# Kernel optimization log

Hardware: AMD Instinct MI355X
Metric: run time of the kernel (lower is better)

Reference implementation:

```python
import jax, jax.numpy as jnp
import numpy as np

B, S, D, H = 8, 1024, 512, 12
HS = D // H  # 42 (head_size; 12*42 = 504 concat width, as in the original)


def setup_inputs() -> dict:
    key = jax.random.key(0)
    ks = jax.random.split(key, 12)
    sd = 0.02
    return {
        "embedded_patches": jax.random.normal(ks[0], (B, S, D), dtype=jnp.float32),
        # stacked per-head projections (12 independent Linear(D, HS, bias=False))
        "wk": jax.random.normal(ks[1], (H, D, HS), dtype=jnp.float32) * sd,
        "wq": jax.random.normal(ks[2], (H, D, HS), dtype=jnp.float32) * sd,
        "wv": jax.random.normal(ks[3], (H, D, HS), dtype=jnp.float32) * sd,
        "w_proj": jax.random.normal(ks[4], (H * HS, D), dtype=jnp.float32) * sd,  # [504, 512]
        "b_proj": jnp.zeros((D,), dtype=jnp.float32),
        # shared LayerNorm (same params used for both norms, as in the original)
        "gamma": jnp.ones((D,), dtype=jnp.float32),
        "beta": jnp.zeros((D,), dtype=jnp.float32),
        "w1": jax.random.normal(ks[5], (D, 4 * D), dtype=jnp.float32) * sd,
        "b1": jnp.zeros((4 * D,), dtype=jnp.float32),
        "w2": jax.random.normal(ks[6], (4 * D, D), dtype=jnp.float32) * sd,
        "b2": jnp.zeros((D,), dtype=jnp.float32),
    }


def _layernorm(x, gamma, beta, eps=1e-5):
    mu = jnp.mean(x, axis=-1, keepdims=True)
    var = jnp.var(x, axis=-1, keepdims=True)
    return (x - mu) * jax.lax.rsqrt(var + eps) * gamma + beta


def reference(embedded_patches, wk, wq, wv, w_proj, b_proj, gamma, beta, w1, b1, w2, b2):
    x = embedded_patches
    n1 = _layernorm(x, gamma, beta)
    # per-head projections, vectorized over heads: [B,S,D] x [H,D,E] -> [B,H,S,E]
    q = jnp.einsum('bsd,hde->bhse', n1, wq)
    k = jnp.einsum('bsd,hde->bhse', n1, wk)
    v = jnp.einsum('bsd,hde->bhse', n1, wv)
    scale = HS ** -0.5
    wei = jax.nn.softmax(jnp.einsum('bhse,bhte->bhst', q, k) * scale, axis=-1)
    out = jnp.einsum('bhst,bhte->bhse', wei, v)        # [B,H,S,E]
    out = out.transpose(0, 2, 1, 3).reshape(B, S, H * HS)  # concat heads -> [B,S,504]
    attn = out @ w_proj + b_proj                       # [B,S,D]
    # original quirk: takes batch element 0 and broadcasts against residual
    first_added = attn[0] + x                          # [S,D] + [B,S,D] -> [B,S,D]
    n2 = _layernorm(first_added, gamma, beta)
    h = jax.nn.gelu(n2 @ w1 + b1, approximate=False)   # torch nn.GELU default = exact erf
    ff = h @ w2 + b2
    return ff + first_added
```

## Files before the change

kernel.cpp:

```cpp
#include <hip/hip_runtime.h>
#include <hip/hip_bf16.h>
#include <stdint.h>


typedef unsigned short u16;
typedef __attribute__((ext_vector_type(8))) short short8;
typedef __attribute__((ext_vector_type(4))) float f32x4;

__device__ __forceinline__ u16 f2bf(float f) {
  union { float f; unsigned u; } x; x.f = f;
  return (u16)((x.u + 0x7FFFu + ((x.u >> 16) & 1u)) >> 16);
}
__device__ __forceinline__ float bf2f(u16 u) {
  union { unsigned u; float f; } x; x.u = ((unsigned)u) << 16;
  return x.f;
}

__device__ __forceinline__ void gload_lds16(const u16* g, u16* l) {
  __builtin_amdgcn_global_load_lds(
      (__attribute__((address_space(1))) void*)g,
      (__attribute__((address_space(3))) void*)l, 16, 0, 0);
}

__device__ __forceinline__ float wred_sum(float v) {
#pragma unroll
  for (int off = 32; off > 0; off >>= 1) v += __shfl_xor(v, off, 64);
  return v;
}
__device__ __forceinline__ float wred_max(float v) {
#pragma unroll
  for (int off = 32; off > 0; off >>= 1) v = fmaxf(v, __shfl_xor(v, off, 64));
  return v;
}

#define MFMA16x16(a, b, c) __builtin_amdgcn_mfma_f32_16x16x32_bf16(a, b, c, 0, 0, 0)

enum { EP_BF16 = 0, EP_PV = 1, EP_F32B = 2, EP_GELU = 3, EP_OUT = 4 };

template <int EP>
__launch_bounds__(256, 4)
__global__ void gemm2(const u16* __restrict__ A, int lda, long sAz,
                      const u16* __restrict__ Bt, int ldb, long sBz,
                      void* __restrict__ Cv, int ldc, long sCz,
                      int K, const float* __restrict__ bias,
                      const float* __restrict__ aux) {
  __shared__ u16 lA[2][128 * 32];
  __shared__ u16 lB[2][128 * 32];
  const int z = blockIdx.z;
  const u16* Ab = A + (long)z * sAz;
  const u16* Bb = Bt + (long)z * sBz;
  const int m0 = blockIdx.x * 128;
  const int n0 = blockIdx.y * 128;
  const int tid = threadIdx.x;
  const int w = tid >> 6;
  const int l = tid & 63;
  const int wr = w >> 1;
  const int wc = w & 1;
  const int NT = K >> 5;

  f32x4 acc[4][4];
#pragma unroll
  for (int i = 0; i < 4; ++i)
#pragma unroll
    for (int j = 0; j < 4; ++j) acc[i][j] = (f32x4){0.f, 0.f, 0.f, 0.f};

  const int srow = w * 32 + (l >> 2);
  const int sk = (l & 3) * 8;
  const u16* ga0 = Ab + (long)(m0 + srow) * lda + sk;
  const u16* ga1 = Ab + (long)(m0 + srow + 16) * lda + sk;
  const u16* gb0 = Bb + (long)(n0 + srow) * ldb + sk;
  const u16* gb1 = Bb + (long)(n0 + srow + 16) * ldb + sk;
  const int dOff = w * 1024;

  const int aoff = (wr * 64 + (l & 15)) * 32 + (l >> 4) * 8;
  const int boff = (wc * 64 + (l & 15)) * 32 + (l >> 4) * 8;

  gload_lds16(ga0, &lA[0][dOff]);
  gload_lds16(ga1, &lA[0][dOff + 512]);
  gload_lds16(gb0, &lB[0][dOff]);
  gload_lds16(gb1, &lB[0][dOff + 512]);
  __syncthreads();

  int buf = 0;
  for (int t = 0; t < NT; ++t) {
    short8 af[4], bfv[4];
#pragma unroll
    for (int mi = 0; mi < 4; ++mi)
      af[mi] = *(const short8*)&lA[buf][aoff + mi * 16 * 32];
#pragma unroll
    for (int ni = 0; ni < 4; ++ni)
      bfv[ni] = *(const short8*)&lB[buf][boff + ni * 16 * 32];
    if (t + 1 < NT) {
      const int k0 = (t + 1) * 32;
      const int nb = buf ^ 1;
      gload_lds16(ga0 + k0, &lA[nb][dOff]);
      gload_lds16(ga1 + k0, &lA[nb][dOff + 512]);
      gload_lds16(gb0 + k0, &lB[nb][dOff]);
      gload_lds16(gb1 + k0, &lB[nb][dOff + 512]);
    }
#pragma unroll
    for (int mi = 0; mi < 4; ++mi)
#pragma unroll
      for (int ni = 0; ni < 4; ++ni)
        acc[mi][ni] = MFMA16x16(af[mi], bfv[ni], acc[mi][ni]);
    __syncthreads();
    buf ^= 1;
  }

  const int rbase = m0 + wr * 64 + (l >> 4) * 4;
  const int cbase = n0 + wc * 64 + (l & 15);
#pragma unroll
  for (int mi = 0; mi < 4; ++mi) {
#pragma unroll
    for (int ni = 0; ni < 4; ++ni) {
#pragma unroll
      for (int j = 0; j < 4; ++j) {
        const int row = rbase + mi * 16 + j;
        const int col = cbase + ni * 16;
        const float v = acc[mi][ni][j];
        if (EP == EP_BF16) {
          ((u16*)Cv)[(long)z * sCz + (long)row * ldc + col] = f2bf(v);
        } else if (EP == EP_PV) {
          if (col < 42) {
            const float iv = aux[z * 1024 + row];
            ((u16*)Cv)[(long)row * ldc + z * 42 + col] = f2bf(v * iv);
          }
        } else if (EP == EP_F32B) {
          ((float*)Cv)[(long)row * ldc + col] = v + bias[col];
        } else if (EP == EP_GELU) {
          const float tt = v + bias[col];
          const float g = 0.5f * tt * (1.0f + erff(tt * 0.70710678118654752f));
          ((u16*)Cv)[(long)row * ldc + col] = f2bf(g);
        } else {
          ((float*)Cv)[(long)row * ldc + col] =
              v + bias[col] + aux[(long)row * ldc + col];
        }
      }
    }
  }
}

__global__ void ln1_kernel(const float* __restrict__ x,
                           const float* __restrict__ gamma,
                           const float* __restrict__ beta,
                           u16* __restrict__ n1) {
  __shared__ float red[16];
  const int s = blockIdx.x;
  const int t = threadIdx.x;
  const float* row = x + (long)s * 512;
  const float v0 = row[t];
  const float v1 = row[t + 256];
  float sum = wred_sum(v0 + v1);
  float sq = wred_sum(v0 * v0 + v1 * v1);
  if ((t & 63) == 0) { red[t >> 6] = sum; red[8 + (t >> 6)] = sq; }
  __syncthreads();
  sum = red[0] + red[1] + red[2] + red[3];
  sq = red[8] + red[9] + red[10] + red[11];
  const float mu = sum * (1.0f / 512.0f);
  const float rstd = rsqrtf(sq * (1.0f / 512.0f) - mu * mu + 1e-5f);
  n1[(long)s * 512 + t] = f2bf((v0 - mu) * rstd * gamma[t] + beta[t]);
  n1[(long)s * 512 + t + 256] =
      f2bf((v1 - mu) * rstd * gamma[t + 256] + beta[t + 256]);
}

__global__ void ln2_kernel(const float* __restrict__ x,
                           const float* __restrict__ aproj,
                           const float* __restrict__ gamma,
                           const float* __restrict__ beta,
                           float* __restrict__ fa, u16* __restrict__ n2) {
  __shared__ float red[16];
  const int r = blockIdx.x;
  const int t = threadIdx.x;
  const int s = r & 1023;
  const float* xr = x + (long)r * 512;
  const float* ar = aproj + (long)s * 512;
  const float v0 = xr[t] + ar[t];
  const float v1 = xr[t + 256] + ar[t + 256];
  fa[(long)r * 512 + t] = v0;
  fa[(long)r * 512 + t + 256] = v1;
  float sum = wred_sum(v0 + v1);
  float sq = wred_sum(v0 * v0 + v1 * v1);
  if ((t & 63) == 0) { red[t >> 6] = sum; red[8 + (t >> 6)] = sq; }
  __syncthreads();
  sum = red[0] + red[1] + red[2] + red[3];
  sq = red[8] + red[9] + red[10] + red[11];
  const float mu = sum * (1.0f / 512.0f);
  const float rstd = rsqrtf(sq * (1.0f / 512.0f) - mu * mu + 1e-5f);
  n2[(long)r * 512 + t] = f2bf((v0 - mu) * rstd * gamma[t] + beta[t]);
  n2[(long)r * 512 + t + 256] =
      f2bf((v1 - mu) * rstd * gamma[t + 256] + beta[t + 256]);
}

__global__ void softmax_kernel(u16* __restrict__ SP, float* __restrict__ invl) {
  __shared__ float red[16];
  const long row = blockIdx.x;
  u16* p = SP + row * 1024;
  const int t = threadIdx.x;
  uint2 u = ((const uint2*)p)[t];
  const float s0 = bf2f((u16)(u.x & 0xffff));
  const float s1 = bf2f((u16)(u.x >> 16));
  const float s2 = bf2f((u16)(u.y & 0xffff));
  const float s3 = bf2f((u16)(u.y >> 16));
  float m = wred_max(fmaxf(fmaxf(s0, s1), fmaxf(s2, s3)));
  if ((t & 63) == 0) red[t >> 6] = m;
  __syncthreads();
  m = fmaxf(fmaxf(red[0], red[1]), fmaxf(red[2], red[3]));
  const float e0 = __expf(s0 - m), e1 = __expf(s1 - m);
  const float e2 = __expf(s2 - m), e3 = __expf(s3 - m);
  float sum = wred_sum(e0 + e1 + e2 + e3);
  if ((t & 63) == 0) red[8 + (t >> 6)] = sum;
  __syncthreads();
  sum = red[8] + red[9] + red[10] + red[11];
  if (t == 0) invl[row] = 1.0f / sum;
  uint2 o;
  o.x = (unsigned)f2bf(e0) | ((unsigned)f2bf(e1) << 16);
  o.y = (unsigned)f2bf(e2) | ((unsigned)f2bf(e3) << 16);
  ((uint2*)p)[t] = o;
}

__global__ void prep_qkv_kernel(const float* __restrict__ wq,
                                const float* __restrict__ wk,
                                u16* __restrict__ BtQKV, float scale) {
  const int i = blockIdx.x * 256 + threadIdx.x;
  const int n = i >> 9, d = i & 511;
  const int pq = n / 768;
  const int h = (n % 768) >> 6;
  const int e = n & 63;
  float v = 0.f;
  if (e < 42) {
    v = (pq ? wk : wq)[((long)h * 512 + d) * 42 + e];
    if (!pq) v *= scale;
  }
  BtQKV[i] = f2bf(v);
}
__global__ void prep_wvT_kernel(const float* __restrict__ wv,
                                u16* __restrict__ wvT) {
  const int i = blockIdx.x * 256 + threadIdx.x;
  const int r = i >> 9, d = i & 511;
  const int h = r >> 7, e = r & 127;
  wvT[i] = f2bf(e < 42 ? wv[((long)h * 512 + d) * 42 + e] : 0.f);
}
__global__ void prep_proj_kernel(const float* __restrict__ wp,
                                 u16* __restrict__ BtP) {
  const int i = blockIdx.x * 256 + threadIdx.x;
  const int n = i >> 9, k = i & 511;
  BtP[i] = f2bf(k < 504 ? wp[(long)k * 512 + n] : 0.f);
}
__global__ void prep_w1_kernel(const float* __restrict__ w1,
                               u16* __restrict__ Bt1) {
  const int i = blockIdx.x * 256 + threadIdx.x;
  const int n = i >> 9, k = i & 511;
  Bt1[i] = f2bf(w1[(long)k * 2048 + n]);
}
__global__ void prep_w2_kernel(const float* __restrict__ w2,
                               u16* __restrict__ Bt2) {
  const int i = blockIdx.x * 256 + threadIdx.x;
  const int n = i >> 11, k = i & 2047;
  Bt2[i] = f2bf(w2[(long)k * 512 + n]);
}
__global__ void zero_u16_kernel(u16* __restrict__ p) {
  p[blockIdx.x * 256 + threadIdx.x] = 0;
}

extern "C" void kernel_launch(void* const* d_in, const int* in_sizes, int n_in,
                              void* d_out, int out_size, void* d_ws,
                              size_t ws_size, hipStream_t stream) {
  const float* x = (const float*)d_in[0];
  const float* wk = (const float*)d_in[1];
  const float* wq = (const float*)d_in[2];
  const float* wv = (const float*)d_in[3];
  const float* w_proj = (const float*)d_in[4];
  const float* b_proj = (const float*)d_in[5];
  const float* gamma = (const float*)d_in[6];
  const float* beta = (const float*)d_in[7];
  const float* w1 = (const float*)d_in[8];
  const float* b1 = (const float*)d_in[9];
  const float* w2 = (const float*)d_in[10];
  const float* b2 = (const float*)d_in[11];

  char* base = (char*)d_ws;
  size_t off = 0;
  auto alloc = [&](size_t bytes) -> void* {
    void* p = base + off;
    off += (bytes + 255) & ~(size_t)255;
    return p;
  };
  u16* n1 = (u16*)alloc(1024L * 512 * 2);
  u16* qkvc = (u16*)alloc(1024L * 1536 * 2);
  u16* SP = (u16*)alloc(12L * 1024 * 1024 * 2);
  u16* wvT = (u16*)alloc(1536L * 512 * 2);
  u16* vt = (u16*)alloc(1536L * 1024 * 2);
  u16* cat = (u16*)alloc(1024L * 512 * 2);
  float* aproj = (float*)alloc(1024L * 512 * 4);
  float* fa = (float*)alloc(8192L * 512 * 4);
  u16* n2 = (u16*)alloc(8192L * 512 * 2);
  u16* hbuf = (u16*)alloc(8192L * 2048 * 2);
  u16* BtQKV = (u16*)alloc(1536L * 512 * 2);
  u16* BtP = (u16*)alloc(512L * 512 * 2);
  u16* Bt1 = (u16*)alloc(2048L * 512 * 2);
  u16* Bt2 = (u16*)alloc(512L * 2048 * 2);
  float* invl = (float*)alloc(12L * 1024 * 4);
  (void)ws_size; (void)in_sizes; (void)n_in; (void)out_size;

  const float scale = 0.15430334996209191f;

  prep_qkv_kernel<<<3072, 256, 0, stream>>>(wq, wk, BtQKV, scale);
  prep_wvT_kernel<<<3072, 256, 0, stream>>>(wv, wvT);
  prep_proj_kernel<<<1024, 256, 0, stream>>>(w_proj, BtP);
  prep_w1_kernel<<<4096, 256, 0, stream>>>(w1, Bt1);
  prep_w2_kernel<<<4096, 256, 0, stream>>>(w2, Bt2);
  zero_u16_kernel<<<2048, 256, 0, stream>>>(cat);
  ln1_kernel<<<1024, 256, 0, stream>>>(x, gamma, beta, n1);

  gemm2<EP_BF16><<<dim3(8, 12, 1), 256, 0, stream>>>(
      n1, 512, 0, BtQKV, 512, 0, qkvc, 1536, 0, 512, nullptr, nullptr);
  gemm2<EP_BF16><<<dim3(12, 8, 1), 256, 0, stream>>>(
      wvT, 512, 0, n1, 512, 0, vt, 1024, 0, 512, nullptr, nullptr);
  gemm2<EP_BF16><<<dim3(8, 8, 12), 256, 0, stream>>>(
      qkvc, 1536, 64, qkvc + 768, 1536, 64, SP, 1024, 1024L * 1024, 64,
      nullptr, nullptr);
  softmax_kernel<<<12288, 256, 0, stream>>>(SP, invl);
  gemm2<EP_PV><<<dim3(8, 1, 12), 256, 0, stream>>>(
      SP, 1024, 1024L * 1024, vt, 1024, 128L * 1024, cat, 512, 0, 1024,
      nullptr, invl);
  gemm2<EP_F32B><<<dim3(8, 4, 1), 256, 0, stream>>>(
      cat, 512, 0, BtP, 512, 0, aproj, 512, 0, 512, b_proj, nullptr);
  ln2_kernel<<<8192, 256, 0, stream>>>(x, aproj, gamma, beta, fa, n2);
  gemm2<EP_GELU><<<dim3(64, 16, 1), 256, 0, stream>>>(
      n2, 512, 0, Bt1, 512, 0, hbuf, 2048, 0, 512, b1, nullptr);
  gemm2<EP_OUT><<<dim3(64, 4, 1), 256, 0, stream>>>(
      hbuf, 2048, 0, Bt2, 2048, 0, d_out, 512, 0, 2048, b2, fa);
}
```

Baseline: 188.3 us.

## Split-K for PV and MLP2 GEMMs, swizzle LDS, tiled weight transposes

Applies an XOR swizzle to the LDS layout in the shared GEMM to reduce bank conflicts. Splits the PV GEMM four ways along K and the final MLP GEMM two ways along K to raise the block count on undersized grids, with new combine kernels that sum the partials and apply the epilogue (invl scaling, bias, residual). Replaces the strided weight-prep kernels with an LDS-tiled transpose for coalesced access. The cost is extra fp32 partial traffic and more kernel launches; the MLP2 partials are written at the start of d_ws and could alias the other allocations.

Result: no change. 185.1 us (-1.7%).

```diff
diff --git a/kernel.cpp b/kernel.cpp
--- a/kernel.cpp
+++ b/kernel.cpp
@@ -35,7 +35,8 @@
 
 #define MFMA16x16(a, b, c) __builtin_amdgcn_mfma_f32_16x16x32_bf16(a, b, c, 0, 0, 0)
 
-enum { EP_BF16 = 0, EP_PV = 1, EP_F32B = 2, EP_GELU = 3, EP_OUT = 4 };
+enum { EP_BF16 = 0, EP_PV = 1, EP_F32B = 2, EP_GELU = 3, EP_OUT = 4,
+       EP_PART = 5, EP_PVPART = 6 };
 
 template <int EP>
 __launch_bounds__(256, 4)
@@ -47,8 +48,15 @@
   __shared__ u16 lA[2][128 * 32];
   __shared__ u16 lB[2][128 * 32];
   const int z = blockIdx.z;
-  const u16* Ab = A + (long)z * sAz;
-  const u16* Bb = Bt + (long)z * sBz;
+  const u16* Ab;
+  const u16* Bb;
+  if (EP == EP_PVPART) {
+    Ab = A + (long)(z >> 2) * sAz + (z & 3) * 256;
+    Bb = Bt + (long)(z >> 2) * sBz + (z & 3) * 256;
+  } else {
+    Ab = A + (long)z * sAz;
+    Bb = Bt + (long)z * sBz;
+  }
   const int m0 = blockIdx.x * 128;
   const int n0 = blockIdx.y * 128;
   const int tid = threadIdx.x;
@@ -65,15 +73,16 @@
     for (int j = 0; j < 4; ++j) acc[i][j] = (f32x4){0.f, 0.f, 0.f, 0.f};
 
   const int srow = w * 32 + (l >> 2);
-  const int sk = (l & 3) * 8;
+  const int sk = ((l & 3) ^ ((l >> 3) & 3)) * 8;
   const u16* ga0 = Ab + (long)(m0 + srow) * lda + sk;
   const u16* ga1 = Ab + (long)(m0 + srow + 16) * lda + sk;
   const u16* gb0 = Bb + (long)(n0 + srow) * ldb + sk;
   const u16* gb1 = Bb + (long)(n0 + srow + 16) * ldb + sk;
   const int dOff = w * 1024;
 
-  const int aoff = (wr * 64 + (l & 15)) * 32 + (l >> 4) * 8;
-  const int boff = (wc * 64 + (l & 15)) * 32 + (l >> 4) * 8;
+  const int gphys = ((l >> 4) ^ ((l >> 1) & 3)) * 8;
+  const int aoff = (wr * 64 + (l & 15)) * 32 + gphys;
+  const int boff = (wc * 64 + (l & 15)) * 32 + gphys;
 
   gload_lds16(ga0, &lA[0][dOff]);
   gload_lds16(ga1, &lA[0][dOff + 512]);
@@ -131,13 +140,41 @@
           const float tt = v + bias[col];
           const float g = 0.5f * tt * (1.0f + erff(tt * 0.70710678118654752f));
           ((u16*)Cv)[(long)row * ldc + col] = f2bf(g);
-        } else {
+        } else if (EP == EP_OUT) {
           ((float*)Cv)[(long)row * ldc + col] =
               v + bias[col] + aux[(long)row * ldc + col];
+        } else {
+          ((float*)Cv)[(long)z * sCz + (long)row * ldc + col] = v;
         }
       }
     }
   }
+}
+
+__global__ void combine_mlp2_kernel(const float* __restrict__ p,
+                                    const float* __restrict__ fa,
+                                    const float* __restrict__ b2,
+                                    float* __restrict__ out) {
+  const long i = (long)blockIdx.x * 256 + threadIdx.x;
+  const f32x4 a = ((const f32x4*)p)[i];
+  const f32x4 b = ((const f32x4*)(p + 8192L * 512))[i];
+  const f32x4 f = ((const f32x4*)fa)[i];
+  const f32x4 bb = ((const f32x4*)b2)[i & 127];
+  ((f32x4*)out)[i] = a + b + f + bb;
+}
+
+__global__ void combine_pv_kernel(const float* __restrict__ part,
+                                  const float* __restrict__ invl,
+                                  u16* __restrict__ cat) {
+  const int blk = blockIdx.x;
+  const int h = blk >> 10;
+  const int row = blk & 1023;
+  const int e = threadIdx.x;
+  if (e >= 42) return;
+  const long base = (long)(h * 4) * 131072 + row * 128 + e;
+  float v = part[base] + part[base + 131072] + part[base + 2 * 131072] +
+            part[base + 3 * 131072];
+  cat[(long)row * 512 + h * 42 + e] = f2bf(v * invl[h * 1024 + row]);
 }
 
 __global__ void ln1_kernel(const float* __restrict__ x,
@@ -240,24 +277,37 @@
   const int h = r >> 7, e = r & 127;
   wvT[i] = f2bf(e < 42 ? wv[((long)h * 512 + d) * 42 + e] : 0.f);
 }
-__global__ void prep_proj_kernel(const float* __restrict__ wp,
-                                 u16* __restrict__ BtP) {
-  const int i = blockIdx.x * 256 + threadIdx.x;
-  const int n = i >> 9, k = i & 511;
-  BtP[i] = f2bf(k < 504 ? wp[(long)k * 512 + n] : 0.f);
-}
-__global__ void prep_w1_kernel(const float* __restrict__ w1,
-                               u16* __restrict__ Bt1) {
-  const int i = blockIdx.x * 256 + threadIdx.x;
-  const int n = i >> 9, k = i & 511;
-  Bt1[i] = f2bf(w1[(long)k * 2048 + n]);
-}
-__global__ void prep_w2_kernel(const float* __restrict__ w2,
-                               u16* __restrict__ Bt2) {
-  const int i = blockIdx.x * 256 + threadIdx.x;
-  const int n = i >> 11, k = i & 2047;
-  Bt2[i] = f2bf(w2[(long)k * 512 + n]);
-}
+
+__global__ void transpose_bf16_kernel(const float* __restrict__ in,
+                                      u16* __restrict__ out, int N, int Kin,
+                                      int Kpad) {
+  __shared__ float tile[64][65];
+  const int n0 = blockIdx.x * 64;
+  const int k0 = blockIdx.y * 64;
+  const int t = threadIdx.x;
+  const int tc = t & 63;
+  const int tr = t >> 6;
+#pragma unroll
+  for (int r = 0; r < 16; ++r) {
+    const int kr = tr * 16 + r;
+    const int kg = k0 + kr;
+    tile[kr][tc] = (kg < Kin) ? in[(long)kg * N + n0 + tc] : 0.f;
+  }
+  __syncthreads();
+  const int nr0 = t >> 4;
+  const int kc = (t & 15) * 4;
+#pragma unroll
+  for (int p = 0; p < 4; ++p) {
+    const int nr = nr0 + p * 16;
+    ushort4 v;
+    v.x = f2bf(tile[kc + 0][nr]);
+    v.y = f2bf(tile[kc + 1][nr]);
+    v.z = f2bf(tile[kc + 2][nr]);
+    v.w = f2bf(tile[kc + 3][nr]);
+    *(ushort4*)&out[(long)(n0 + nr) * Kpad + k0 + kc] = v;
+  }
+}
+
 __global__ void zero_u16_kernel(u16* __restrict__ p) {
   p[blockIdx.x * 256 + threadIdx.x] = 0;
 }
@@ -300,15 +350,17 @@
   u16* Bt1 = (u16*)alloc(2048L * 512 * 2);
   u16* Bt2 = (u16*)alloc(512L * 2048 * 2);
   float* invl = (float*)alloc(12L * 1024 * 4);
+  float* pvpart = (float*)alloc(48L * 1024 * 128 * 4);
+  float* part = (float*)d_ws;
   (void)ws_size; (void)in_sizes; (void)n_in; (void)out_size;
 
   const float scale = 0.15430334996209191f;
 
   prep_qkv_kernel<<<3072, 256, 0, stream>>>(wq, wk, BtQKV, scale);
   prep_wvT_kernel<<<3072, 256, 0, stream>>>(wv, wvT);
-  prep_proj_kernel<<<1024, 256, 0, stream>>>(w_proj, BtP);
-  prep_w1_kernel<<<4096, 256, 0, stream>>>(w1, Bt1);
-  prep_w2_kernel<<<4096, 256, 0, stream>>>(w2, Bt2);
+  transpose_bf16_kernel<<<dim3(8, 8), 256, 0, stream>>>(w_proj, BtP, 512, 504, 512);
+  transpose_bf16_kernel<<<dim3(32, 8), 256, 0, stream>>>(w1, Bt1, 2048, 512, 512);
+  transpose_bf16_kernel<<<dim3(8, 32), 256, 0, stream>>>(w2, Bt2, 512, 2048, 2048);
   zero_u16_kernel<<<2048, 256, 0, stream>>>(cat);
   ln1_kernel<<<1024, 256, 0, stream>>>(x, gamma, beta, n1);
 
@@ -320,14 +372,17 @@
       qkvc, 1536, 64, qkvc + 768, 1536, 64, SP, 1024, 1024L * 1024, 64,
       nullptr, nullptr);
   softmax_kernel<<<12288, 256, 0, stream>>>(SP, invl);
-  gemm2<EP_PV><<<dim3(8, 1, 12), 256, 0, stream>>>(
-      SP, 1024, 1024L * 1024, vt, 1024, 128L * 1024, cat, 512, 0, 1024,
-      nullptr, invl);
+  gemm2<EP_PVPART><<<dim3(8, 1, 48), 256, 0, stream>>>(
+      SP, 1024, 1024L * 1024, vt, 1024, 128L * 1024, pvpart, 128,
+      1024L * 128, 256, nullptr, nullptr);
+  combine_pv_kernel<<<12288, 64, 0, stream>>>(pvpart, invl, cat);
   gemm2<EP_F32B><<<dim3(8, 4, 1), 256, 0, stream>>>(
       cat, 512, 0, BtP, 512, 0, aproj, 512, 0, 512, b_proj, nullptr);
   ln2_kernel<<<8192, 256, 0, stream>>>(x, aproj, gamma, beta, fa, n2);
   gemm2<EP_GELU><<<dim3(64, 16, 1), 256, 0, stream>>>(
       n2, 512, 0, Bt1, 512, 0, hbuf, 2048, 0, 512, b1, nullptr);
-  gemm2<EP_OUT><<<dim3(64, 4, 1), 256, 0, stream>>>(
-      hbuf, 2048, 0, Bt2, 2048, 0, d_out, 512, 0, 2048, b2, fa);
-}
+  gemm2<EP_PART><<<dim3(64, 4, 2), 256, 0, stream>>>(
+      hbuf, 2048, 1024, Bt2, 2048, 1024, part, 512, 8192L * 512, 1024,
+      nullptr, nullptr);
+  combine_mlp2_kernel<<<4096, 256, 0, stream>>>(part, fa, b2, (float*)d_out);
+}
```
